# Kernel optimization log

Hardware: AMD Instinct MI355X
Metric: run time of the kernel (lower is better)

The kernel has to match this reference:

```python
import jax, jax.numpy as jnp
import numpy as np

R = 2            # radix
N = 1024         # input_size (power of R)
DEPTH = 10       # log_R(N) levels
SIZES = [N >> l for l in range(DEPTH)]                 # per-level input_size: 1024,512,...,2
OFFSETS = np.concatenate([[0], np.cumsum(SIZES)])      # offsets into flat butterfly-weight vector
TOTAL_W = int(OFFSETS[-1])                             # 2046
# residual cascade in the torch code: int(True)-1 = 0 (False), int(0)-1 = -1 -> bool(-1)=True,
# and it stays truthy for all deeper levels.
RES = [True, False] + [True] * (DEPTH - 2)


def setup_inputs() -> dict:
    key = jax.random.key(0)
    k1, k2, k3 = jax.random.split(key, 3)
    x = jax.random.normal(k1, (4, 4096, N), dtype=jnp.float32)
    bw = jax.random.normal(k2, (TOTAL_W,), dtype=jnp.float32) * 0.1   # xavier-ish scale
    lw = jax.random.normal(k3, (DEPTH, R, R), dtype=jnp.float32) * 0.5
    return {"x": x, "bw": bw, "lw": lw}


def _fft(x, bw, lw, level):
    """One DIT radix-R butterfly level applied to the last dim of x (eval mode: dropout = id)."""
    n = x.shape[-1]                                   # input_size at this level
    o = int(OFFSETS[level])
    w = bw[o:o + n].reshape(R, n // R)                # elementwise 'twiddle' weights (r, n/r)
    xr = x.reshape(x.shape[:-1] + (R, n // R))        # (..., r, n/r)
    inner = _fft(xr, bw, lw, level + 1) if n > R else xr   # recurse on last dim n/r; Identity at base
    # torch: einsum('ij,...ik->...jk', lin_weights, weights * recursive(x))
    y = jnp.einsum('ij,...ik->...jk', lw[level], w * inner).reshape(x.shape)
    return x + y if RES[level] else y


def reference(x, bw, lw):
    return _fft(x, bw, lw, 0)
```

## Files before the change

### kernel.cpp

```cpp
#include <hip/hip_runtime.h>


constexpr int VECLEN = 1024;

__device__ __forceinline__ int swz(int f) {
  return f ^ (((f >> 5) & 7) << 2);
}

template<int L, bool RESL>
__device__ __forceinline__ void level_inlane(float (&v)[16], const float (&xr)[16],
                                             const float* __restrict__ bw,
                                             const float* __restrict__ lw) {
  constexpr int n = VECLEN >> L;
  constexpr int h = n >> 1;
  constexpr int off = 2048 - (2048 >> L);
  float w[n];
#pragma unroll
  for (int i = 0; i < n; ++i) w[i] = bw[off + i];
  const float l00 = lw[L*4+0], l01 = lw[L*4+1], l10 = lw[L*4+2], l11 = lw[L*4+3];
#pragma unroll
  for (int r = 0; r < 16; ++r) {
    if ((r & h) == 0) {
      const int q = r ^ h;
      const float t0 = w[r & (n-1)] * v[r];
      const float t1 = w[q & (n-1)] * v[q];
      const float y0 = l00*t0 + l10*t1;
      const float y1 = l01*t0 + l11*t1;
      v[r] = RESL ? xr[r] + y0 : y0;
      v[q] = RESL ? xr[q] + y1 : y1;
    }
  }
}

template<int L, bool RESL>
__device__ __forceinline__ void level_dpp(float (&v)[16], const float (&xr)[16],
                                          const float (&w)[16],
                                          const float* __restrict__ lw, int lane) {
  static_assert(L == 4 || L == 5, "DPP levels only");
  const int role = (lane >> (5 - L)) & 1;
  const float l00 = lw[L*4+0], l01 = lw[L*4+1], l10 = lw[L*4+2], l11 = lw[L*4+3];
  const float cs = role ? l11 : l00;
  const float cp = role ? l01 : l10;
#pragma unroll
  for (int r = 0; r < 16; ++r) {
    const float t = w[r] * v[r];
    const int ti = __float_as_int(t);
    const int pi = (L == 5)
      ? __builtin_amdgcn_update_dpp(0, ti, 0xB1, 0xF, 0xF, true)
      : __builtin_amdgcn_update_dpp(0, ti, 0x4E, 0xF, 0xF, true);
    const float tp = __int_as_float(pi);
    const float y = cs*t + cp*tp;
    v[r] = RESL ? xr[r] + y : y;
  }
}

template<int L>
__device__ __forceinline__ void loadw_A(float (&w)[16], const float* lds_bw, int lane) {
  constexpr int n = VECLEN >> L;
  constexpr int off = 2048 - (2048 >> L);
  const int f0 = off + ((lane * 16) & (n - 1));
#pragma unroll
  for (int k = 0; k < 4; ++k) {
    const float4 f = *reinterpret_cast<const float4*>(lds_bw + swz(f0 + 4*k));
    w[4*k+0]=f.x; w[4*k+1]=f.y; w[4*k+2]=f.z; w[4*k+3]=f.w;
  }
}

template<int L>
__device__ __forceinline__ void loadw_B(float* w, const float* lds_bw, int lane) {
  constexpr int off = 2048 - (2048 >> L);
  constexpr int nr = (VECLEN >> L) >> 6;
#pragma unroll
  for (int j = 0; j < nr; ++j)
    w[j] = lds_bw[swz(off + j*64 + lane)];
}

template<int L, bool RESL>
__device__ __forceinline__ void level_B(float (&v)[16], const float (&xr)[16],
                                        const float* w, const float* __restrict__ lw) {
  constexpr int nr = (VECLEN >> L) >> 6;
  constexpr int hb = nr >> 1;
  const float l00 = lw[L*4+0], l01 = lw[L*4+1], l10 = lw[L*4+2], l11 = lw[L*4+3];
#pragma unroll
  for (int r = 0; r < 16; ++r) {
    if ((r & hb) == 0) {
      const int q = r ^ hb;
      const float t0 = w[r & (nr-1)] * v[r];
      const float t1 = w[q & (nr-1)] * v[q];
      const float y0 = l00*t0 + l10*t1;
      const float y1 = l01*t0 + l11*t1;
      v[r] = RESL ? xr[r] + y0 : y0;
      v[q] = RESL ? xr[q] + y1 : y1;
    }
  }
}

__global__ __launch_bounds__(256)
void rnnfft_kernel(const float* __restrict__ x,
                   const float* __restrict__ bw,
                   const float* __restrict__ lw,
                   float* __restrict__ out, int nvec) {
  __shared__ float lds_bw[2048];
  __shared__ float tbuf[4][1024];
  const int t = threadIdx.x;
  const int w4 = t >> 6;
  const int lane = t & 63;
  const int wid = blockIdx.x * 4 + w4;
  const size_t base = (size_t)wid * VECLEN;

  float v[16], xrA[16], xrB[16];
#pragma unroll
  for (int k = 0; k < 4; ++k) {
    const float4 f = *reinterpret_cast<const float4*>(x + base + lane*16 + 4*k);
    xrA[4*k+0]=f.x; xrA[4*k+1]=f.y; xrA[4*k+2]=f.z; xrA[4*k+3]=f.w;
  }
#pragma unroll
  for (int r = 0; r < 16; ++r) xrB[r] = x[base + r*64 + lane];

  if (t < 252) {
    const float4 a = *reinterpret_cast<const float4*>(bw + 8*t);
    const float4 b = *reinterpret_cast<const float4*>(bw + 8*t + 4);
    *reinterpret_cast<float4*>(lds_bw + swz(8*t)) = a;
    *reinterpret_cast<float4*>(lds_bw + swz(8*t+4)) = b;
  }
  __syncthreads();

#pragma unroll
  for (int r = 0; r < 16; ++r) v[r] = xrA[r];

  float wA[16], wB[16];
  loadw_A<5>(wA, lds_bw, lane);
  loadw_A<4>(wB, lds_bw, lane);

  level_inlane<9, true>(v, xrA, bw, lw);
  level_inlane<8, true>(v, xrA, bw, lw);
  level_inlane<7, true>(v, xrA, bw, lw);
  level_inlane<6, true>(v, xrA, bw, lw);
  level_dpp<5, true>(v, xrA, wA, lw, lane);
  level_dpp<4, true>(v, xrA, wB, lw, lane);

  float* buf = tbuf[w4];
#pragma unroll
  for (int k = 0; k < 4; ++k) {
    float4 f;
    f.x = v[4*k+0]; f.y = v[4*k+1]; f.z = v[4*k+2]; f.w = v[4*k+3];
    *reinterpret_cast<float4*>(buf + swz(lane*16 + 4*k)) = f;
  }
  float w3[2], w2[4], w1[8], w0[16];
  loadw_B<3>(w3, lds_bw, lane);
  loadw_B<2>(w2, lds_bw, lane);
#pragma unroll
  for (int r = 0; r < 16; ++r) v[r] = buf[swz(r*64 + lane)];

  level_B<3, true >(v, xrB, w3, lw);
  loadw_B<1>(w1, lds_bw, lane);
  level_B<2, true >(v, xrB, w2, lw);
  loadw_B<0>(w0, lds_bw, lane);
  level_B<1, false>(v, xrB, w1, lw);
  level_B<0, true >(v, xrB, w0, lw);

#pragma unroll
  for (int r = 0; r < 16; ++r) out[base + r*64 + lane] = v[r];
}

extern "C" void kernel_launch(void* const* d_in, const int* in_sizes, int n_in,
                              void* d_out, int out_size, void* d_ws, size_t ws_size,
                              hipStream_t stream) {
  const float* x  = (const float*)d_in[0];
  const float* bw = (const float*)d_in[1];
  const float* lw = (const float*)d_in[2];
  float* out = (float*)d_out;
  const int nvec = in_sizes[0] / VECLEN;
  const int wpb = 4;
  const int blocks = (nvec + wpb - 1) / wpb;
  rnnfft_kernel<<<blocks, 256, 0, stream>>>(x, bw, lw, out, nvec);
}
```

Baseline: 31.05 us.

## Process two vectors per wavefront to amortize twiddle loads and overheads

Measured after the change: 36.48 us. 17.5% more time.

```diff
diff --git a/kernel.cpp b/kernel.cpp
--- a/kernel.cpp
+++ b/kernel.cpp
@@ -7,8 +7,10 @@
   return f ^ (((f >> 5) & 7) << 2);
 }
 
+struct f2 { float x, y; };
+
 template<int L, bool RESL>
-__device__ __forceinline__ void level_inlane(float (&v)[16], const float (&xr)[16],
+__device__ __forceinline__ void level_inlane(f2 (&v)[16], const f2 (&xr)[16],
                                              const float* __restrict__ bw,
                                              const float* __restrict__ lw) {
   constexpr int n = VECLEN >> L;
@@ -22,35 +24,37 @@
   for (int r = 0; r < 16; ++r) {
     if ((r & h) == 0) {
       const int q = r ^ h;
-      const float t0 = w[r & (n-1)] * v[r];
-      const float t1 = w[q & (n-1)] * v[q];
-      const float y0 = l00*t0 + l10*t1;
-      const float y1 = l01*t0 + l11*t1;
-      v[r] = RESL ? xr[r] + y0 : y0;
-      v[q] = RESL ? xr[q] + y1 : y1;
+      const float w0 = w[r & (n-1)], w1 = w[q & (n-1)];
+      const float t0x = w0*v[r].x, t0y = w0*v[r].y;
+      const float t1x = w1*v[q].x, t1y = w1*v[q].y;
+      const float y0x = l00*t0x + l10*t1x, y0y = l00*t0y + l10*t1y;
+      const float y1x = l01*t0x + l11*t1x, y1y = l01*t0y + l11*t1y;
+      v[r].x = RESL ? xr[r].x + y0x : y0x;  v[r].y = RESL ? xr[r].y + y0y : y0y;
+      v[q].x = RESL ? xr[q].x + y1x : y1x;  v[q].y = RESL ? xr[q].y + y1y : y1y;
     }
   }
 }
 
 template<int L, bool RESL>
-__device__ __forceinline__ void level_dpp(float (&v)[16], const float (&xr)[16],
+__device__ __forceinline__ void level_dpp(f2 (&v)[16], const f2 (&xr)[16],
                                           const float (&w)[16],
                                           const float* __restrict__ lw, int lane) {
   static_assert(L == 4 || L == 5, "DPP levels only");
+  constexpr int ctl = (L == 5) ? 0xB1 : 0x4E;
   const int role = (lane >> (5 - L)) & 1;
   const float l00 = lw[L*4+0], l01 = lw[L*4+1], l10 = lw[L*4+2], l11 = lw[L*4+3];
   const float cs = role ? l11 : l00;
   const float cp = role ? l01 : l10;
 #pragma unroll
   for (int r = 0; r < 16; ++r) {
-    const float t = w[r] * v[r];
-    const int ti = __float_as_int(t);
-    const int pi = (L == 5)
-      ? __builtin_amdgcn_update_dpp(0, ti, 0xB1, 0xF, 0xF, true)
-      : __builtin_amdgcn_update_dpp(0, ti, 0x4E, 0xF, 0xF, true);
-    const float tp = __int_as_float(pi);
-    const float y = cs*t + cp*tp;
-    v[r] = RESL ? xr[r] + y : y;
+    const float tx = w[r] * v[r].x, ty = w[r] * v[r].y;
+    const float px = __int_as_float(
+        __builtin_amdgcn_update_dpp(0, __float_as_int(tx), ctl, 0xF, 0xF, true));
+    const float py = __int_as_float(
+        __builtin_amdgcn_update_dpp(0, __float_as_int(ty), ctl, 0xF, 0xF, true));
+    const float yx = cs*tx + cp*px, yy = cs*ty + cp*py;
+    v[r].x = RESL ? xr[r].x + yx : yx;
+    v[r].y = RESL ? xr[r].y + yy : yy;
   }
 }
 
@@ -76,7 +80,7 @@
 }
 
 template<int L, bool RESL>
-__device__ __forceinline__ void level_B(float (&v)[16], const float (&xr)[16],
+__device__ __forceinline__ void level_B(f2 (&v)[16], const f2 (&xr)[16],
                                         const float* w, const float* __restrict__ lw) {
   constexpr int nr = (VECLEN >> L) >> 6;
   constexpr int hb = nr >> 1;
@@ -85,37 +89,39 @@
   for (int r = 0; r < 16; ++r) {
     if ((r & hb) == 0) {
       const int q = r ^ hb;
-      const float t0 = w[r & (nr-1)] * v[r];
-      const float t1 = w[q & (nr-1)] * v[q];
-      const float y0 = l00*t0 + l10*t1;
-      const float y1 = l01*t0 + l11*t1;
-      v[r] = RESL ? xr[r] + y0 : y0;
-      v[q] = RESL ? xr[q] + y1 : y1;
+      const float w0 = w[r & (nr-1)], w1 = w[q & (nr-1)];
+      const float t0x = w0*v[r].x, t0y = w0*v[r].y;
+      const float t1x = w1*v[q].x, t1y = w1*v[q].y;
+      const float y0x = l00*t0x + l10*t1x, y0y = l00*t0y + l10*t1y;
+      const float y1x = l01*t0x + l11*t1x, y1y = l01*t0y + l11*t1y;
+      v[r].x = RESL ? xr[r].x + y0x : y0x;  v[r].y = RESL ? xr[r].y + y0y : y0y;
+      v[q].x = RESL ? xr[q].x + y1x : y1x;  v[q].y = RESL ? xr[q].y + y1y : y1y;
     }
   }
 }
 
 __global__ __launch_bounds__(256)
+__attribute__((amdgpu_waves_per_eu(4)))
 void rnnfft_kernel(const float* __restrict__ x,
                    const float* __restrict__ bw,
                    const float* __restrict__ lw,
                    float* __restrict__ out, int nvec) {
   __shared__ float lds_bw[2048];
-  __shared__ float tbuf[4][1024];
+  __shared__ float tbuf[4][2][1024];
   const int t = threadIdx.x;
   const int w4 = t >> 6;
   const int lane = t & 63;
   const int wid = blockIdx.x * 4 + w4;
-  const size_t base = (size_t)wid * VECLEN;
+  const size_t base = (size_t)wid * (2 * VECLEN);
 
-  float v[16], xrA[16], xrB[16];
+  f2 v[16], xrA[16];
 #pragma unroll
   for (int k = 0; k < 4; ++k) {
-    const float4 f = *reinterpret_cast<const float4*>(x + base + lane*16 + 4*k);
-    xrA[4*k+0]=f.x; xrA[4*k+1]=f.y; xrA[4*k+2]=f.z; xrA[4*k+3]=f.w;
+    const float4 a = *reinterpret_cast<const float4*>(x + base + lane*16 + 4*k);
+    const float4 b = *reinterpret_cast<const float4*>(x + base + VECLEN + lane*16 + 4*k);
+    xrA[4*k+0] = {a.x, b.x}; xrA[4*k+1] = {a.y, b.y};
+    xrA[4*k+2] = {a.z, b.z}; xrA[4*k+3] = {a.w, b.w};
   }
-#pragma unroll
-  for (int r = 0; r < 16; ++r) xrB[r] = x[base + r*64 + lane];
 
   if (t < 252) {
     const float4 a = *reinterpret_cast<const float4*>(bw + 8*t);
@@ -139,18 +145,28 @@
   level_dpp<5, true>(v, xrA, wA, lw, lane);
   level_dpp<4, true>(v, xrA, wB, lw, lane);
 
-  float* buf = tbuf[w4];
+  float* b0 = tbuf[w4][0];
+  float* b1 = tbuf[w4][1];
 #pragma unroll
   for (int k = 0; k < 4; ++k) {
-    float4 f;
-    f.x = v[4*k+0]; f.y = v[4*k+1]; f.z = v[4*k+2]; f.w = v[4*k+3];
-    *reinterpret_cast<float4*>(buf + swz(lane*16 + 4*k)) = f;
+    float4 fx, fy;
+    fx.x = v[4*k+0].x; fx.y = v[4*k+1].x; fx.z = v[4*k+2].x; fx.w = v[4*k+3].x;
+    fy.x = v[4*k+0].y; fy.y = v[4*k+1].y; fy.z = v[4*k+2].y; fy.w = v[4*k+3].y;
+    *reinterpret_cast<float4*>(b0 + swz(lane*16 + 4*k)) = fx;
+    *reinterpret_cast<float4*>(b1 + swz(lane*16 + 4*k)) = fy;
   }
+
+  f2 xrB[16];
+#pragma unroll
+  for (int r = 0; r < 16; ++r)
+    xrB[r] = { x[base + r*64 + lane], x[base + VECLEN + r*64 + lane] };
+
   float w3[2], w2[4], w1[8], w0[16];
   loadw_B<3>(w3, lds_bw, lane);
   loadw_B<2>(w2, lds_bw, lane);
 #pragma unroll
-  for (int r = 0; r < 16; ++r) v[r] = buf[swz(r*64 + lane)];
+  for (int r = 0; r < 16; ++r)
+    v[r] = { b0[swz(r*64 + lane)], b1[swz(r*64 + lane)] };
 
   level_B<3, true >(v, xrB, w3, lw);
   loadw_B<1>(w1, lds_bw, lane);
@@ -160,7 +176,10 @@
   level_B<0, true >(v, xrB, w0, lw);
 
 #pragma unroll
-  for (int r = 0; r < 16; ++r) out[base + r*64 + lane] = v[r];
+  for (int r = 0; r < 16; ++r) {
+    out[base + r*64 + lane] = v[r].x;
+    out[base + VECLEN + r*64 + lane] = v[r].y;
+  }
 }
 
 extern "C" void kernel_launch(void* const* d_in, const int* in_sizes, int n_in,
@@ -171,7 +190,8 @@
   const float* lw = (const float*)d_in[2];
   float* out = (float*)d_out;
   const int nvec = in_sizes[0] / VECLEN;
+  const int nwave = nvec / 2;
   const int wpb = 4;
-  const int blocks = (nvec + wpb - 1) / wpb;
+  const int blocks = (nwave + wpb - 1) / wpb;
   rnnfft_kernel<<<blocks, 256, 0, stream>>>(x, bw, lw, out, nvec);
 }
```

## Process two vectors per wave with prefetch of the second vector's input

Applied to the files above, without the earlier changes.

Result: no change. 31.12 us (+0.2%).

```diff
diff --git a/kernel.cpp b/kernel.cpp
--- a/kernel.cpp
+++ b/kernel.cpp
@@ -37,6 +37,7 @@
                                           const float (&w)[16],
                                           const float* __restrict__ lw, int lane) {
   static_assert(L == 4 || L == 5, "DPP levels only");
+  constexpr int ctl = (L == 5) ? 0xB1 : 0x4E;
   const int role = (lane >> (5 - L)) & 1;
   const float l00 = lw[L*4+0], l01 = lw[L*4+1], l10 = lw[L*4+2], l11 = lw[L*4+3];
   const float cs = role ? l11 : l00;
@@ -44,11 +45,8 @@
 #pragma unroll
   for (int r = 0; r < 16; ++r) {
     const float t = w[r] * v[r];
-    const int ti = __float_as_int(t);
-    const int pi = (L == 5)
-      ? __builtin_amdgcn_update_dpp(0, ti, 0xB1, 0xF, 0xF, true)
-      : __builtin_amdgcn_update_dpp(0, ti, 0x4E, 0xF, 0xF, true);
-    const float tp = __int_as_float(pi);
+    const float tp = __int_as_float(
+        __builtin_amdgcn_update_dpp(0, __float_as_int(t), ctl, 0xF, 0xF, true));
     const float y = cs*t + cp*tp;
     v[r] = RESL ? xr[r] + y : y;
   }
@@ -95,7 +93,52 @@
   }
 }
 
+__device__ __forceinline__ void phaseA(float (&v)[16], const float (&xrA)[16],
+                                       const float* lds_bw,
+                                       const float* __restrict__ bw,
+                                       const float* __restrict__ lw, int lane) {
+  float wA[16], wB[16];
+  loadw_A<5>(wA, lds_bw, lane);
+  loadw_A<4>(wB, lds_bw, lane);
+  level_inlane<9, true>(v, xrA, bw, lw);
+  level_inlane<8, true>(v, xrA, bw, lw);
+  level_inlane<7, true>(v, xrA, bw, lw);
+  level_inlane<6, true>(v, xrA, bw, lw);
+  level_dpp<5, true>(v, xrA, wA, lw, lane);
+  level_dpp<4, true>(v, xrA, wB, lw, lane);
+}
+
+__device__ __forceinline__ void phaseB(float (&v)[16], const float (&xrB)[16],
+                                       const float* lds_bw,
+                                       const float* __restrict__ lw, int lane) {
+  float w3[2], w2[4], w1[8], w0[16];
+  loadw_B<3>(w3, lds_bw, lane);
+  loadw_B<2>(w2, lds_bw, lane);
+  level_B<3, true >(v, xrB, w3, lw);
+  loadw_B<1>(w1, lds_bw, lane);
+  level_B<2, true >(v, xrB, w2, lw);
+  loadw_B<0>(w0, lds_bw, lane);
+  level_B<1, false>(v, xrB, w1, lw);
+  level_B<0, true >(v, xrB, w0, lw);
+}
+
+__device__ __forceinline__ void loadX_A(float (&xr)[16], const float* __restrict__ x,
+                                        size_t base, int lane) {
+#pragma unroll
+  for (int k = 0; k < 4; ++k) {
+    const float4 f = *reinterpret_cast<const float4*>(x + base + lane*16 + 4*k);
+    xr[4*k+0]=f.x; xr[4*k+1]=f.y; xr[4*k+2]=f.z; xr[4*k+3]=f.w;
+  }
+}
+
+__device__ __forceinline__ void loadX_B(float (&xr)[16], const float* __restrict__ x,
+                                        size_t base, int lane) {
+#pragma unroll
+  for (int r = 0; r < 16; ++r) xr[r] = x[base + r*64 + lane];
+}
+
 __global__ __launch_bounds__(256)
+__attribute__((amdgpu_waves_per_eu(3)))
 void rnnfft_kernel(const float* __restrict__ x,
                    const float* __restrict__ bw,
                    const float* __restrict__ lw,
@@ -106,16 +149,13 @@
   const int w4 = t >> 6;
   const int lane = t & 63;
   const int wid = blockIdx.x * 4 + w4;
-  const size_t base = (size_t)wid * VECLEN;
+  const size_t baseA = (size_t)(2 * wid) * VECLEN;
+  const size_t baseB = baseA + VECLEN;
+  float* buf = tbuf[w4];
 
   float v[16], xrA[16], xrB[16];
-#pragma unroll
-  for (int k = 0; k < 4; ++k) {
-    const float4 f = *reinterpret_cast<const float4*>(x + base + lane*16 + 4*k);
-    xrA[4*k+0]=f.x; xrA[4*k+1]=f.y; xrA[4*k+2]=f.z; xrA[4*k+3]=f.w;
-  }
-#pragma unroll
-  for (int r = 0; r < 16; ++r) xrB[r] = x[base + r*64 + lane];
+  loadX_A(xrA, x, baseA, lane);
+  loadX_B(xrB, x, baseA, lane);
 
   if (t < 252) {
     const float4 a = *reinterpret_cast<const float4*>(bw + 8*t);
@@ -127,40 +167,39 @@
 
 #pragma unroll
   for (int r = 0; r < 16; ++r) v[r] = xrA[r];
-
-  float wA[16], wB[16];
-  loadw_A<5>(wA, lds_bw, lane);
-  loadw_A<4>(wB, lds_bw, lane);
-
-  level_inlane<9, true>(v, xrA, bw, lw);
-  level_inlane<8, true>(v, xrA, bw, lw);
-  level_inlane<7, true>(v, xrA, bw, lw);
-  level_inlane<6, true>(v, xrA, bw, lw);
-  level_dpp<5, true>(v, xrA, wA, lw, lane);
-  level_dpp<4, true>(v, xrA, wB, lw, lane);
-
-  float* buf = tbuf[w4];
+  phaseA(v, xrA, lds_bw, bw, lw, lane);
+
 #pragma unroll
   for (int k = 0; k < 4; ++k) {
     float4 f;
     f.x = v[4*k+0]; f.y = v[4*k+1]; f.z = v[4*k+2]; f.w = v[4*k+3];
     *reinterpret_cast<float4*>(buf + swz(lane*16 + 4*k)) = f;
   }
-  float w3[2], w2[4], w1[8], w0[16];
-  loadw_B<3>(w3, lds_bw, lane);
-  loadw_B<2>(w2, lds_bw, lane);
+  loadX_A(xrA, x, baseB, lane);
+
 #pragma unroll
   for (int r = 0; r < 16; ++r) v[r] = buf[swz(r*64 + lane)];
-
-  level_B<3, true >(v, xrB, w3, lw);
-  loadw_B<1>(w1, lds_bw, lane);
-  level_B<2, true >(v, xrB, w2, lw);
-  loadw_B<0>(w0, lds_bw, lane);
-  level_B<1, false>(v, xrB, w1, lw);
-  level_B<0, true >(v, xrB, w0, lw);
-
-#pragma unroll
-  for (int r = 0; r < 16; ++r) out[base + r*64 + lane] = v[r];
+  phaseB(v, xrB, lds_bw, lw, lane);
+#pragma unroll
+  for (int r = 0; r < 16; ++r) out[baseA + r*64 + lane] = v[r];
+
+  loadX_B(xrB, x, baseB, lane);
+
+#pragma unroll
+  for (int r = 0; r < 16; ++r) v[r] = xrA[r];
+  phaseA(v, xrA, lds_bw, bw, lw, lane);
+
+#pragma unroll
+  for (int k = 0; k < 4; ++k) {
+    float4 f;
+    f.x = v[4*k+0]; f.y = v[4*k+1]; f.z = v[4*k+2]; f.w = v[4*k+3];
+    *reinterpret_cast<float4*>(buf + swz(lane*16 + 4*k)) = f;
+  }
+#pragma unroll
+  for (int r = 0; r < 16; ++r) v[r] = buf[swz(r*64 + lane)];
+  phaseB(v, xrB, lds_bw, lw, lane);
+#pragma unroll
+  for (int r = 0; r < 16; ++r) out[baseB + r*64 + lane] = v[r];
 }
 
 extern "C" void kernel_launch(void* const* d_in, const int* in_sizes, int n_in,
@@ -171,7 +210,8 @@
   const float* lw = (const float*)d_in[2];
   float* out = (float*)d_out;
   const int nvec = in_sizes[0] / VECLEN;
+  const int nwave = nvec / 2;
   const int wpb = 4;
-  const int blocks = (nvec + wpb - 1) / wpb;
+  const int blocks = (nwave + wpb - 1) / wpb;
   rnnfft_kernel<<<blocks, 256, 0, stream>>>(x, bw, lw, out, nvec);
 }
```

## Split each 1024-vector across two waves with 8 elements per lane

Applied to the files above, without the earlier changes.

Result: slower. 32.36 us (+4.2%).

```diff
diff --git a/kernel.cpp b/kernel.cpp
--- a/kernel.cpp
+++ b/kernel.cpp
@@ -8,9 +8,9 @@
 }
 
 template<int L, bool RESL>
-__device__ __forceinline__ void level_inlane(float (&v)[16], const float (&xr)[16],
-                                             const float* __restrict__ bw,
-                                             const float* __restrict__ lw) {
+__device__ __forceinline__ void level_inA(float (&v)[8], const float (&xr)[8],
+                                          const float* __restrict__ bw,
+                                          const float* __restrict__ lw) {
   constexpr int n = VECLEN >> L;
   constexpr int h = n >> 1;
   constexpr int off = 2048 - (2048 >> L);
@@ -19,7 +19,7 @@
   for (int i = 0; i < n; ++i) w[i] = bw[off + i];
   const float l00 = lw[L*4+0], l01 = lw[L*4+1], l10 = lw[L*4+2], l11 = lw[L*4+3];
 #pragma unroll
-  for (int r = 0; r < 16; ++r) {
+  for (int r = 0; r < 8; ++r) {
     if ((r & h) == 0) {
       const int q = r ^ h;
       const float t0 = w[r & (n-1)] * v[r];
@@ -33,64 +33,74 @@
 }
 
 template<int L, bool RESL>
-__device__ __forceinline__ void level_dpp(float (&v)[16], const float (&xr)[16],
-                                          const float (&w)[16],
-                                          const float* __restrict__ lw, int lane) {
-  static_assert(L == 4 || L == 5, "DPP levels only");
-  const int role = (lane >> (5 - L)) & 1;
+__device__ __forceinline__ void level_x(float (&v)[8], const float (&xr)[8],
+                                        const float (&w)[8],
+                                        const float* __restrict__ lw, int lane) {
+  static_assert(L >= 3 && L <= 6, "cross levels");
+  const int role = (lane >> (6 - L)) & 1;
   const float l00 = lw[L*4+0], l01 = lw[L*4+1], l10 = lw[L*4+2], l11 = lw[L*4+3];
   const float cs = role ? l11 : l00;
   const float cp = role ? l01 : l10;
 #pragma unroll
-  for (int r = 0; r < 16; ++r) {
+  for (int r = 0; r < 8; ++r) {
     const float t = w[r] * v[r];
     const int ti = __float_as_int(t);
-    const int pi = (L == 5)
-      ? __builtin_amdgcn_update_dpp(0, ti, 0xB1, 0xF, 0xF, true)
-      : __builtin_amdgcn_update_dpp(0, ti, 0x4E, 0xF, 0xF, true);
+    int pi;
+    if constexpr (L == 6) pi = __builtin_amdgcn_update_dpp(0, ti, 0xB1, 0xF, 0xF, true);
+    else if constexpr (L == 5) pi = __builtin_amdgcn_update_dpp(0, ti, 0x4E, 0xF, 0xF, true);
+    else if constexpr (L == 4) pi = __builtin_amdgcn_ds_swizzle(ti, 0x101F);
+    else pi = __builtin_amdgcn_ds_swizzle(ti, 0x201F);
     const float tp = __int_as_float(pi);
     const float y = cs*t + cp*tp;
     v[r] = RESL ? xr[r] + y : y;
   }
 }
 
-template<int L>
-__device__ __forceinline__ void loadw_A(float (&w)[16], const float* lds_bw, int lane) {
-  constexpr int n = VECLEN >> L;
-  constexpr int off = 2048 - (2048 >> L);
-  const int f0 = off + ((lane * 16) & (n - 1));
-#pragma unroll
-  for (int k = 0; k < 4; ++k) {
-    const float4 f = *reinterpret_cast<const float4*>(lds_bw + swz(f0 + 4*k));
-    w[4*k+0]=f.x; w[4*k+1]=f.y; w[4*k+2]=f.z; w[4*k+3]=f.w;
-  }
+__device__ __forceinline__ void loadw6(float (&w)[8], const float* __restrict__ bw,
+                                       int lane) {
+  const int b = 2016 + (lane & 1) * 8;
+  const float4 f0 = *reinterpret_cast<const float4*>(bw + b);
+  const float4 f1 = *reinterpret_cast<const float4*>(bw + b + 4);
+  w[0]=f0.x; w[1]=f0.y; w[2]=f0.z; w[3]=f0.w;
+  w[4]=f1.x; w[5]=f1.y; w[6]=f1.z; w[7]=f1.w;
 }
 
 template<int L>
-__device__ __forceinline__ void loadw_B(float* w, const float* lds_bw, int lane) {
+__device__ __forceinline__ void loadwX(float (&w)[8], const float* lds_bw, int lane) {
+  constexpr int n = VECLEN >> L;
   constexpr int off = 2048 - (2048 >> L);
-  constexpr int nr = (VECLEN >> L) >> 6;
+  const int b = off + ((lane * 8) & (n - 1));
+  const float4 f0 = *reinterpret_cast<const float4*>(lds_bw + swz(b));
+  const float4 f1 = *reinterpret_cast<const float4*>(lds_bw + swz(b + 4));
+  w[0]=f0.x; w[1]=f0.y; w[2]=f0.z; w[3]=f0.w;
+  w[4]=f1.x; w[5]=f1.y; w[6]=f1.z; w[7]=f1.w;
+}
+
+template<int L>
+__device__ __forceinline__ void loadwB(float* w, const float* lds_bw, int gl) {
+  constexpr int off = 2048 - (2048 >> L);
+  constexpr int nw = (VECLEN >> L) >> 7;
 #pragma unroll
-  for (int j = 0; j < nr; ++j)
-    w[j] = lds_bw[swz(off + j*64 + lane)];
+  for (int j = 0; j < nw; ++j)
+    w[j] = lds_bw[swz(off + j*128 + gl)];
 }
 
 template<int L, bool RESL>
-__device__ __forceinline__ void level_B(float (&v)[16], const float (&xr)[16],
+__device__ __forceinline__ void level_B(float (&v)[8], const float (&xr)[8],
                                         const float* w, const float* __restrict__ lw) {
-  constexpr int nr = (VECLEN >> L) >> 6;
-  constexpr int hb = nr >> 1;
+  constexpr int nw = (VECLEN >> L) >> 7;
+  constexpr int hb = nw >> 1;
   const float l00 = lw[L*4+0], l01 = lw[L*4+1], l10 = lw[L*4+2], l11 = lw[L*4+3];
 #pragma unroll
-  for (int r = 0; r < 16; ++r) {
-    if ((r & hb) == 0) {
-      const int q = r ^ hb;
-      const float t0 = w[r & (nr-1)] * v[r];
-      const float t1 = w[q & (nr-1)] * v[q];
+  for (int rb = 0; rb < 8; ++rb) {
+    if ((rb & hb) == 0) {
+      const int q = rb ^ hb;
+      const float t0 = w[rb & (nw-1)] * v[rb];
+      const float t1 = w[q & (nw-1)] * v[q];
       const float y0 = l00*t0 + l10*t1;
       const float y1 = l01*t0 + l11*t1;
-      v[r] = RESL ? xr[r] + y0 : y0;
-      v[q] = RESL ? xr[q] + y1 : y1;
+      v[rb] = RESL ? xr[rb] + y0 : y0;
+      v[q]  = RESL ? xr[q]  + y1 : y1;
     }
   }
 }
@@ -101,21 +111,22 @@
                    const float* __restrict__ lw,
                    float* __restrict__ out, int nvec) {
   __shared__ float lds_bw[2048];
-  __shared__ float tbuf[4][1024];
+  __shared__ float tbuf[2][1024];
   const int t = threadIdx.x;
-  const int w4 = t >> 6;
   const int lane = t & 63;
-  const int wid = blockIdx.x * 4 + w4;
-  const size_t base = (size_t)wid * VECLEN;
+  const int wv = (t >> 6) & 1;
+  const int p  = t >> 7;
+  const int gl = wv * 64 + lane;
+  const int vid = blockIdx.x * 2 + p;
+  const size_t base = (size_t)vid * VECLEN;
 
-  float v[16], xrA[16], xrB[16];
-#pragma unroll
-  for (int k = 0; k < 4; ++k) {
-    const float4 f = *reinterpret_cast<const float4*>(x + base + lane*16 + 4*k);
-    xrA[4*k+0]=f.x; xrA[4*k+1]=f.y; xrA[4*k+2]=f.z; xrA[4*k+3]=f.w;
+  float v[8], xr[8];
+  {
+    const float4 f0 = *reinterpret_cast<const float4*>(x + base + gl*8);
+    const float4 f1 = *reinterpret_cast<const float4*>(x + base + gl*8 + 4);
+    xr[0]=f0.x; xr[1]=f0.y; xr[2]=f0.z; xr[3]=f0.w;
+    xr[4]=f1.x; xr[5]=f1.y; xr[6]=f1.z; xr[7]=f1.w;
   }
-#pragma unroll
-  for (int r = 0; r < 16; ++r) xrB[r] = x[base + r*64 + lane];
 
   if (t < 252) {
     const float4 a = *reinterpret_cast<const float4*>(bw + 8*t);
@@ -126,41 +137,48 @@
   __syncthreads();
 
 #pragma unroll
-  for (int r = 0; r < 16; ++r) v[r] = xrA[r];
+  for (int r = 0; r < 8; ++r) v[r] = xr[r];
 
-  float wA[16], wB[16];
-  loadw_A<5>(wA, lds_bw, lane);
-  loadw_A<4>(wB, lds_bw, lane);
+  float w6[8], w5[8], w4[8], w3[8];
+  loadw6(w6, bw, lane);
+  loadwX<5>(w5, lds_bw, lane);
+  loadwX<4>(w4, lds_bw, lane);
+  loadwX<3>(w3, lds_bw, lane);
 
-  level_inlane<9, true>(v, xrA, bw, lw);
-  level_inlane<8, true>(v, xrA, bw, lw);
-  level_inlane<7, true>(v, xrA, bw, lw);
-  level_inlane<6, true>(v, xrA, bw, lw);
-  level_dpp<5, true>(v, xrA, wA, lw, lane);
-  level_dpp<4, true>(v, xrA, wB, lw, lane);
+  level_inA<9, true>(v, xr, bw, lw);
+  level_inA<8, true>(v, xr, bw, lw);
+  level_inA<7, true>(v, xr, bw, lw);
+  level_x<6, true>(v, xr, w6, lw, lane);
+  level_x<5, true>(v, xr, w5, lw, lane);
+  level_x<4, true>(v, xr, w4, lw, lane);
+  level_x<3, true>(v, xr, w3, lw, lane);
 
-  float* buf = tbuf[w4];
+  float* buf = tbuf[p];
+  {
+    float4 f0, f1;
+    f0.x=v[0]; f0.y=v[1]; f0.z=v[2]; f0.w=v[3];
+    f1.x=v[4]; f1.y=v[5]; f1.z=v[6]; f1.w=v[7];
+    *reinterpret_cast<float4*>(buf + swz(gl*8))     = f0;
+    *reinterpret_cast<float4*>(buf + swz(gl*8 + 4)) = f1;
+  }
+  float xrB[8];
 #pragma unroll
-  for (int k = 0; k < 4; ++k) {
-    float4 f;
-    f.x = v[4*k+0]; f.y = v[4*k+1]; f.z = v[4*k+2]; f.w = v[4*k+3];
-    *reinterpret_cast<float4*>(buf + swz(lane*16 + 4*k)) = f;
-  }
-  float w3[2], w2[4], w1[8], w0[16];
-  loadw_B<3>(w3, lds_bw, lane);
-  loadw_B<2>(w2, lds_bw, lane);
+  for (int rb = 0; rb < 8; ++rb) xrB[rb] = x[base + rb*128 + gl];
+  float w2[2], w1[4], w0[8];
+  loadwB<2>(w2, lds_bw, gl);
+  loadwB<1>(w1, lds_bw, gl);
+  loadwB<0>(w0, lds_bw, gl);
+  __syncthreads();
+
 #pragma unroll
-  for (int r = 0; r < 16; ++r) v[r] = buf[swz(r*64 + lane)];
+  for (int rb = 0; rb < 8; ++rb) v[rb] = buf[swz(rb*128 + gl)];
 
-  level_B<3, true >(v, xrB, w3, lw);
-  loadw_B<1>(w1, lds_bw, lane);
   level_B<2, true >(v, xrB, w2, lw);
-  loadw_B<0>(w0, lds_bw, lane);
   level_B<1, false>(v, xrB, w1, lw);
   level_B<0, true >(v, xrB, w0, lw);
 
 #pragma unroll
-  for (int r = 0; r < 16; ++r) out[base + r*64 + lane] = v[r];
+  for (int rb = 0; rb < 8; ++rb) out[base + rb*128 + gl] = v[rb];
 }
 
 extern "C" void kernel_launch(void* const* d_in, const int* in_sizes, int n_in,
@@ -171,7 +189,6 @@
   const float* lw = (const float*)d_in[2];
   float* out = (float*)d_out;
   const int nvec = in_sizes[0] / VECLEN;
-  const int wpb = 4;
-  const int blocks = (nvec + wpb - 1) / wpb;
+  const int blocks = nvec / 2;
   rnnfft_kernel<<<blocks, 256, 0, stream>>>(x, bw, lw, out, nvec);
 }
```
